# Kernel optimization log

Hardware: AMD Instinct MI355X
Metric: run time of the kernel (lower is better)

The kernel has to match this reference:

```python
import jax, jax.numpy as jnp
import numpy as np

GAMMA = 0.99  # discount_factor
RHO = 1.0     # rho truncation level
CIS = 1.0     # cis truncation level
T, B = 2048, 8192  # (seq_len, batch)


def setup_inputs() -> dict:
    key = jax.random.key(0)
    k1, k2, k3, k4 = jax.random.split(key, 4)
    return {
        "target_value": jax.random.normal(k1, (T, B), jnp.float32),
        "rewards": jax.random.normal(k2, (T, B), jnp.float32),
        "target_log_policy": jax.random.normal(k3, (T, B), jnp.float32) * 0.1,
        "behaviour_log_policy": jax.random.normal(k4, (T, B), jnp.float32) * 0.1,
    }


def reference(target_value, rewards, target_log_policy, behaviour_log_policy):
    # importance sampling weights, truncated
    is_w = jnp.exp(target_log_policy - behaviour_log_policy)
    rhos = jnp.minimum(RHO, is_w)   # (T, B)
    ciss = jnp.minimum(CIS, is_w)   # (T, B)

    v = target_value
    v_next = v[1:]                  # V(x_{s+1}), (T-1, B)
    # delta_s = rho_s * (r_s + gamma*V(x_{s+1}) - V(x_s))
    delta = rhos[:-1] * (rewards[:-1] + GAMMA * v_next - v[:-1])
    # vtrace_s = a_s + b_s * vtrace_{s+1}, affine recurrence coefficients:
    a = v[:-1] + delta - GAMMA * ciss[:-1] * v_next  # (T-1, B)
    b = GAMMA * ciss[:-1]                             # (T-1, B)

    def step(carry, ab):
        a_i, b_i = ab
        vt = a_i + b_i * carry
        return vt, vt

    last = v[-1]  # vtrace[-1] = V(x_{T-1})
    _, vs = jax.lax.scan(step, last, (a, b), reverse=True)  # (T-1, B)
    vtrace = jnp.concatenate([vs, last[None]], axis=0)      # (T, B)
    return vtrace, rhos
```

## Files before the change

kernel.cpp:

```cpp
#include <hip/hip_runtime.h>

#define T_DIM 2048
#define B_DIM 8192
#define GAMMA 0.99f
#define NCHUNK 256
#define CHUNK_L 8

typedef float v4f __attribute__((ext_vector_type(4)));

__device__ __forceinline__ void nt_store4(float* p, float4 x) {
    __builtin_nontemporal_store(*(v4f*)&x, (v4f*)p);
}

__global__ __launch_bounds__(256) void vtrace_pass1(
    const float* __restrict__ v, const float* __restrict__ rew,
    const float* __restrict__ tlp, const float* __restrict__ blp,
    float* __restrict__ out_a,
    float* __restrict__ out_rho,
    float* __restrict__ Aw, float* __restrict__ Bw)
{
    const int j    = blockIdx.x * blockDim.x + threadIdx.x;
    const int c    = blockIdx.y;
    const int col  = j * 4;
    const int base = c * CHUNK_L * B_DIM + col;

    float4 t4[CHUNK_L], b4[CHUNK_L], v4[CHUNK_L], r4[CHUNK_L];
    #pragma unroll
    for (int r = 0; r < CHUNK_L; ++r)
        t4[r] = *(const float4*)(tlp + base + r * B_DIM);
    #pragma unroll
    for (int r = 0; r < CHUNK_L; ++r)
        b4[r] = *(const float4*)(blp + base + r * B_DIM);
    #pragma unroll
    for (int r = 0; r < CHUNK_L; ++r)
        v4[r] = *(const float4*)(v + base + r * B_DIM);
    #pragma unroll
    for (int r = 0; r < CHUNK_L; ++r)
        r4[r] = *(const float4*)(rew + base + r * B_DIM);

    __builtin_amdgcn_sched_barrier(0);

    const bool last_chunk = (c == NCHUNK - 1);
    float4 rho[CHUNK_L], a4[CHUNK_L], bv[CHUNK_L];
    #pragma unroll
    for (int r = 0; r < CHUNK_L; ++r) {
        rho[r].x = fminf(1.f, __expf(t4[r].x - b4[r].x));
        rho[r].y = fminf(1.f, __expf(t4[r].y - b4[r].y));
        rho[r].z = fminf(1.f, __expf(t4[r].z - b4[r].z));
        rho[r].w = fminf(1.f, __expf(t4[r].w - b4[r].w));
    }
    #pragma unroll
    for (int r = 0; r < CHUNK_L; ++r) {
        if (last_chunk && r == CHUNK_L - 1) {
            a4[r] = v4[r];
            bv[r] = make_float4(0.f, 0.f, 0.f, 0.f);
        } else {
            a4[r].x = fmaf(rho[r].x, r4[r].x - v4[r].x, v4[r].x);
            a4[r].y = fmaf(rho[r].y, r4[r].y - v4[r].y, v4[r].y);
            a4[r].z = fmaf(rho[r].z, r4[r].z - v4[r].z, v4[r].z);
            a4[r].w = fmaf(rho[r].w, r4[r].w - v4[r].w, v4[r].w);
            bv[r].x = GAMMA * rho[r].x;
            bv[r].y = GAMMA * rho[r].y;
            bv[r].z = GAMMA * rho[r].z;
            bv[r].w = GAMMA * rho[r].w;
        }
    }

    float4 A  = make_float4(0.f, 0.f, 0.f, 0.f);
    float4 Bc = make_float4(1.f, 1.f, 1.f, 1.f);
    #pragma unroll
    for (int r = CHUNK_L - 1; r >= 0; --r) {
        A.x = fmaf(bv[r].x, A.x, a4[r].x);
        A.y = fmaf(bv[r].y, A.y, a4[r].y);
        A.z = fmaf(bv[r].z, A.z, a4[r].z);
        A.w = fmaf(bv[r].w, A.w, a4[r].w);
        Bc.x *= bv[r].x; Bc.y *= bv[r].y; Bc.z *= bv[r].z; Bc.w *= bv[r].w;
    }

    #pragma unroll
    for (int r = 0; r < CHUNK_L; ++r)
        *(float4*)(out_rho + base + r * B_DIM) = rho[r];
    #pragma unroll
    for (int r = 0; r < CHUNK_L; ++r)
        *(float4*)(out_a + base + r * B_DIM) = a4[r];

    const int widx = c * B_DIM + col;
    *(float4*)(Aw + widx) = A;
    *(float4*)(Bw + widx) = Bc;
}

__global__ __launch_bounds__(256) void vtrace_carry(
    const float* __restrict__ Aw, const float* __restrict__ Bw,
    float* __restrict__ cb)
{
    const int j = blockIdx.x * blockDim.x + threadIdx.x;
    float x = 0.f;
    #pragma unroll 8
    for (int c = NCHUNK - 1; c >= 0; --c) {
        const int i = c * B_DIM + j;
        const float Av = Aw[i];
        const float Bv = Bw[i];
        cb[i] = x;
        x = fmaf(Bv, x, Av);
    }
}

__global__ __launch_bounds__(256) void vtrace_apply(
    float* __restrict__ out_v,
    const float* __restrict__ rho_arr,
    const float* __restrict__ cb)
{
    const int j   = blockIdx.x * blockDim.x + threadIdx.x;
    const int c   = blockIdx.y;
    const int col = j * 4;
    const int t_hi = (c + 1) * CHUNK_L - 1;
    const int t_lo = c * CHUNK_L;

    float4 carry = *(const float4*)(cb + c * B_DIM + col);

    int idx = t_hi * B_DIM + col;
    #pragma unroll
    for (int t = t_hi; t >= t_lo; --t, idx -= B_DIM) {
        const float4 a4  = *(const float4*)(out_v   + idx);
        const float4 rho = *(const float4*)(rho_arr + idx);
        const float g = (t == T_DIM - 1) ? 0.f : GAMMA;
        float4 o;
        o.x = fmaf(g * rho.x, carry.x, a4.x);
        o.y = fmaf(g * rho.y, carry.y, a4.y);
        o.z = fmaf(g * rho.z, carry.z, a4.z);
        o.w = fmaf(g * rho.w, carry.w, a4.w);
        nt_store4(out_v + idx, o);
        carry = o;
    }
}

extern "C" void kernel_launch(void* const* d_in, const int* in_sizes, int n_in,
                              void* d_out, int out_size, void* d_ws, size_t ws_size,
                              hipStream_t stream) {
    const float* v   = (const float*)d_in[0];
    const float* rew = (const float*)d_in[1];
    const float* tlp = (const float*)d_in[2];
    const float* blp = (const float*)d_in[3];

    float* out_v   = (float*)d_out;
    float* out_rho = out_v + (size_t)T_DIM * B_DIM;

    float* Aw = (float*)d_ws;
    float* Bw = Aw + (size_t)NCHUNK * B_DIM;
    float* cb = Bw + (size_t)NCHUNK * B_DIM;

    dim3 blk(256);
    dim3 grid_scan(B_DIM / 4 / 256, NCHUNK);

    vtrace_pass1<<<grid_scan, blk, 0, stream>>>(v, rew, tlp, blp,
                                                out_v, out_rho, Aw, Bw);
    vtrace_carry<<<dim3(B_DIM / 256), blk, 0, stream>>>(Aw, Bw, cb);
    vtrace_apply<<<grid_scan, blk, 0, stream>>>(out_v, out_rho, cb);
}
```

Before: 125.9 us.

## Recompute recurrence coefficients in apply pass instead of storing intermediate a

The first pass no longer writes the affine coefficient array a; it only writes rho (now with nontemporal stores) and the per-chunk summaries. The apply pass re-reads the four raw inputs, recomputes rho and a, and runs the chunk scan from the carry. This removes one intermediate write and two intermediate reads, but adds four input reads in the second pass, so total memory traffic may rise unless the inputs stay cached.

Result: slower. 129.8 us (+3.1%).

```diff
diff --git a/kernel.cpp b/kernel.cpp
--- a/kernel.cpp
+++ b/kernel.cpp
@@ -15,7 +15,6 @@
 __global__ __launch_bounds__(256) void vtrace_pass1(
     const float* __restrict__ v, const float* __restrict__ rew,
     const float* __restrict__ tlp, const float* __restrict__ blp,
-    float* __restrict__ out_a,
     float* __restrict__ out_rho,
     float* __restrict__ Aw, float* __restrict__ Bw)
 {
@@ -23,66 +22,60 @@
     const int c    = blockIdx.y;
     const int col  = j * 4;
     const int base = c * CHUNK_L * B_DIM + col;
+    const bool last_chunk = (c == NCHUNK - 1);
 
-    float4 t4[CHUNK_L], b4[CHUNK_L], v4[CHUNK_L], r4[CHUNK_L];
+    float4 t4[CHUNK_L], b4[CHUNK_L];
     #pragma unroll
     for (int r = 0; r < CHUNK_L; ++r)
         t4[r] = *(const float4*)(tlp + base + r * B_DIM);
     #pragma unroll
     for (int r = 0; r < CHUNK_L; ++r)
         b4[r] = *(const float4*)(blp + base + r * B_DIM);
+    __builtin_amdgcn_sched_barrier(0);
+
+    float4 rho[CHUNK_L];
+    #pragma unroll
+    for (int r = 0; r < CHUNK_L; ++r) {
+        rho[r].x = fminf(1.f, __expf(t4[r].x - b4[r].x));
+        rho[r].y = fminf(1.f, __expf(t4[r].y - b4[r].y));
+        rho[r].z = fminf(1.f, __expf(t4[r].z - b4[r].z));
+        rho[r].w = fminf(1.f, __expf(t4[r].w - b4[r].w));
+        nt_store4(out_rho + base + r * B_DIM, rho[r]);
+    }
+
+    float4 v4[CHUNK_L], r4[CHUNK_L];
     #pragma unroll
     for (int r = 0; r < CHUNK_L; ++r)
         v4[r] = *(const float4*)(v + base + r * B_DIM);
     #pragma unroll
     for (int r = 0; r < CHUNK_L; ++r)
         r4[r] = *(const float4*)(rew + base + r * B_DIM);
-
     __builtin_amdgcn_sched_barrier(0);
-
-    const bool last_chunk = (c == NCHUNK - 1);
-    float4 rho[CHUNK_L], a4[CHUNK_L], bv[CHUNK_L];
-    #pragma unroll
-    for (int r = 0; r < CHUNK_L; ++r) {
-        rho[r].x = fminf(1.f, __expf(t4[r].x - b4[r].x));
-        rho[r].y = fminf(1.f, __expf(t4[r].y - b4[r].y));
-        rho[r].z = fminf(1.f, __expf(t4[r].z - b4[r].z));
-        rho[r].w = fminf(1.f, __expf(t4[r].w - b4[r].w));
-    }
-    #pragma unroll
-    for (int r = 0; r < CHUNK_L; ++r) {
-        if (last_chunk && r == CHUNK_L - 1) {
-            a4[r] = v4[r];
-            bv[r] = make_float4(0.f, 0.f, 0.f, 0.f);
-        } else {
-            a4[r].x = fmaf(rho[r].x, r4[r].x - v4[r].x, v4[r].x);
-            a4[r].y = fmaf(rho[r].y, r4[r].y - v4[r].y, v4[r].y);
-            a4[r].z = fmaf(rho[r].z, r4[r].z - v4[r].z, v4[r].z);
-            a4[r].w = fmaf(rho[r].w, r4[r].w - v4[r].w, v4[r].w);
-            bv[r].x = GAMMA * rho[r].x;
-            bv[r].y = GAMMA * rho[r].y;
-            bv[r].z = GAMMA * rho[r].z;
-            bv[r].w = GAMMA * rho[r].w;
-        }
-    }
 
     float4 A  = make_float4(0.f, 0.f, 0.f, 0.f);
     float4 Bc = make_float4(1.f, 1.f, 1.f, 1.f);
     #pragma unroll
     for (int r = CHUNK_L - 1; r >= 0; --r) {
-        A.x = fmaf(bv[r].x, A.x, a4[r].x);
-        A.y = fmaf(bv[r].y, A.y, a4[r].y);
-        A.z = fmaf(bv[r].z, A.z, a4[r].z);
-        A.w = fmaf(bv[r].w, A.w, a4[r].w);
-        Bc.x *= bv[r].x; Bc.y *= bv[r].y; Bc.z *= bv[r].z; Bc.w *= bv[r].w;
+        float4 a4, bv;
+        if (last_chunk && r == CHUNK_L - 1) {
+            a4 = v4[r];
+            bv = make_float4(0.f, 0.f, 0.f, 0.f);
+        } else {
+            a4.x = fmaf(rho[r].x, r4[r].x - v4[r].x, v4[r].x);
+            a4.y = fmaf(rho[r].y, r4[r].y - v4[r].y, v4[r].y);
+            a4.z = fmaf(rho[r].z, r4[r].z - v4[r].z, v4[r].z);
+            a4.w = fmaf(rho[r].w, r4[r].w - v4[r].w, v4[r].w);
+            bv.x = GAMMA * rho[r].x;
+            bv.y = GAMMA * rho[r].y;
+            bv.z = GAMMA * rho[r].z;
+            bv.w = GAMMA * rho[r].w;
+        }
+        A.x = fmaf(bv.x, A.x, a4.x);
+        A.y = fmaf(bv.y, A.y, a4.y);
+        A.z = fmaf(bv.z, A.z, a4.z);
+        A.w = fmaf(bv.w, A.w, a4.w);
+        Bc.x *= bv.x; Bc.y *= bv.y; Bc.z *= bv.z; Bc.w *= bv.w;
     }
-
-    #pragma unroll
-    for (int r = 0; r < CHUNK_L; ++r)
-        *(float4*)(out_rho + base + r * B_DIM) = rho[r];
-    #pragma unroll
-    for (int r = 0; r < CHUNK_L; ++r)
-        *(float4*)(out_a + base + r * B_DIM) = a4[r];
 
     const int widx = c * B_DIM + col;
     *(float4*)(Aw + widx) = A;
@@ -106,31 +99,67 @@
 }
 
 __global__ __launch_bounds__(256) void vtrace_apply(
+    const float* __restrict__ v, const float* __restrict__ rew,
+    const float* __restrict__ tlp, const float* __restrict__ blp,
     float* __restrict__ out_v,
-    const float* __restrict__ rho_arr,
     const float* __restrict__ cb)
 {
-    const int j   = blockIdx.x * blockDim.x + threadIdx.x;
-    const int c   = blockIdx.y;
-    const int col = j * 4;
-    const int t_hi = (c + 1) * CHUNK_L - 1;
-    const int t_lo = c * CHUNK_L;
+    const int j    = blockIdx.x * blockDim.x + threadIdx.x;
+    const int c    = blockIdx.y;
+    const int col  = j * 4;
+    const int base = c * CHUNK_L * B_DIM + col;
+    const bool last_chunk = (c == NCHUNK - 1);
 
-    float4 carry = *(const float4*)(cb + c * B_DIM + col);
+    float4 t4[CHUNK_L], b4[CHUNK_L];
+    #pragma unroll
+    for (int r = 0; r < CHUNK_L; ++r)
+        t4[r] = *(const float4*)(tlp + base + r * B_DIM);
+    #pragma unroll
+    for (int r = 0; r < CHUNK_L; ++r)
+        b4[r] = *(const float4*)(blp + base + r * B_DIM);
+    __builtin_amdgcn_sched_barrier(0);
 
-    int idx = t_hi * B_DIM + col;
+    float4 rho[CHUNK_L];
     #pragma unroll
-    for (int t = t_hi; t >= t_lo; --t, idx -= B_DIM) {
-        const float4 a4  = *(const float4*)(out_v   + idx);
-        const float4 rho = *(const float4*)(rho_arr + idx);
-        const float g = (t == T_DIM - 1) ? 0.f : GAMMA;
-        float4 o;
-        o.x = fmaf(g * rho.x, carry.x, a4.x);
-        o.y = fmaf(g * rho.y, carry.y, a4.y);
-        o.z = fmaf(g * rho.z, carry.z, a4.z);
-        o.w = fmaf(g * rho.w, carry.w, a4.w);
-        nt_store4(out_v + idx, o);
-        carry = o;
+    for (int r = 0; r < CHUNK_L; ++r) {
+        rho[r].x = fminf(1.f, __expf(t4[r].x - b4[r].x));
+        rho[r].y = fminf(1.f, __expf(t4[r].y - b4[r].y));
+        rho[r].z = fminf(1.f, __expf(t4[r].z - b4[r].z));
+        rho[r].w = fminf(1.f, __expf(t4[r].w - b4[r].w));
+    }
+
+    float4 v4[CHUNK_L], r4[CHUNK_L];
+    #pragma unroll
+    for (int r = 0; r < CHUNK_L; ++r)
+        v4[r] = *(const float4*)(v + base + r * B_DIM);
+    #pragma unroll
+    for (int r = 0; r < CHUNK_L; ++r)
+        r4[r] = *(const float4*)(rew + base + r * B_DIM);
+    __builtin_amdgcn_sched_barrier(0);
+
+    float4 x = *(const float4*)(cb + c * B_DIM + col);
+
+    #pragma unroll
+    for (int r = CHUNK_L - 1; r >= 0; --r) {
+        float4 a4, bv;
+        if (last_chunk && r == CHUNK_L - 1) {
+            a4 = v4[r];
+            bv = make_float4(0.f, 0.f, 0.f, 0.f);
+        } else {
+            a4.x = fmaf(rho[r].x, r4[r].x - v4[r].x, v4[r].x);
+            a4.y = fmaf(rho[r].y, r4[r].y - v4[r].y, v4[r].y);
+            a4.z = fmaf(rho[r].z, r4[r].z - v4[r].z, v4[r].z);
+            a4.w = fmaf(rho[r].w, r4[r].w - v4[r].w, v4[r].w);
+            bv.x = GAMMA * rho[r].x;
+            bv.y = GAMMA * rho[r].y;
+            bv.z = GAMMA * rho[r].z;
+            bv.w = GAMMA * rho[r].w;
+        }
+        x.x = fmaf(bv.x, x.x, a4.x);
+        x.y = fmaf(bv.y, x.y, a4.y);
+        x.z = fmaf(bv.z, x.z, a4.z);
+        x.w = fmaf(bv.w, x.w, a4.w);
+        nt_store4(out_v + base + r * B_DIM, x);
     }
 }
 
@@ -153,7 +182,8 @@
     dim3 grid_scan(B_DIM / 4 / 256, NCHUNK);
 
     vtrace_pass1<<<grid_scan, blk, 0, stream>>>(v, rew, tlp, blp,
-                                                out_v, out_rho, Aw, Bw);
+                                                out_rho, Aw, Bw);
     vtrace_carry<<<dim3(B_DIM / 256), blk, 0, stream>>>(Aw, Bw, cb);
-    vtrace_apply<<<grid_scan, blk, 0, stream>>>(out_v, out_rho, cb);
+    vtrace_apply<<<grid_scan, blk, 0, stream>>>(v, rew, tlp, blp,
+                                                out_v, cb);
 }
```
